# Kernel optimization log

Hardware: AMD Instinct MI355X
Metric: run time of the kernel (lower is better)

Reference implementation:

```python
import jax, jax.numpy as jnp
import numpy as np

B, N, T, NL, DIM, H, HD = 4, 2048, 8, 64, 1024, 16, 64


def setup_inputs() -> dict:
    key = jax.random.key(0)
    ks = jax.random.split(key, 8)
    text = jax.random.normal(ks[0], (B, N, DIM), dtype=jnp.float32)
    media = jax.random.normal(ks[1], (B, T, NL, DIM), dtype=jnp.float32)
    # place exactly T media tokens per row, evenly spaced, so cumsum times are in [1, T]
    loc = np.zeros((B, N), dtype=bool)
    step = N // T
    loc[:, np.arange(T) * step] = True
    media_locations = jnp.asarray(loc)
    s = 1.0 / np.sqrt(DIM)
    wq = jax.random.normal(ks[2], (DIM, DIM), dtype=jnp.float32) * s
    wkv = jax.random.normal(ks[3], (DIM, 2 * DIM), dtype=jnp.float32) * s
    wo = jax.random.normal(ks[4], (DIM, DIM), dtype=jnp.float32) * s
    bo = jnp.zeros((DIM,), dtype=jnp.float32)
    ln_g = jnp.ones((DIM,), dtype=jnp.float32)
    ln_b = jnp.zeros((DIM,), dtype=jnp.float32)
    return {"text": text, "media": media, "media_locations": media_locations,
            "wq": wq, "wkv": wkv, "wo": wo, "bo": bo, "ln_g": ln_g, "ln_b": ln_b}


def _layernorm(x, g, b, eps=1e-5):
    mu = jnp.mean(x, axis=-1, keepdims=True)
    var = jnp.var(x, axis=-1, keepdims=True)
    return (x - mu) * jax.lax.rsqrt(var + eps) * g + b


def reference(text, media, media_locations, wq, wkv, wo, bo, ln_g, ln_b):
    b, t, nl, d = media.shape
    tn = _layernorm(text, ln_g, ln_b)                 # [b, n, d]
    q = tn @ wq                                        # [b, n, d]
    m = media.reshape(b, t * nl, d)                    # [b, tn, d]
    kv = m @ wkv                                       # [b, tn, 2d]
    k, v = jnp.split(kv, 2, axis=-1)
    q = q.reshape(b, -1, H, HD).transpose(0, 2, 1, 3)  # [b, h, n, hd]
    k = k.reshape(b, -1, H, HD).transpose(0, 2, 1, 3)  # [b, h, tn, hd]
    v = v.reshape(b, -1, H, HD).transpose(0, 2, 1, 3)
    scores = jnp.einsum('bhid,bhjd->bhij', q, k)       # [b, h, n, tn]
    text_times = jnp.cumsum(media_locations.astype(jnp.int32), axis=-1)  # [b, n]
    media_times = jnp.repeat(jnp.arange(1, t + 1, dtype=jnp.int32), nl)  # [tn]
    mask = text_times[:, None, :, None] == media_times[None, None, None, :]
    neg = jnp.finfo(scores.dtype).min
    scores = jnp.where(mask, scores, neg)
    attn = jax.nn.softmax(scores, axis=-1)
    no_media = (text_times == 0)[:, None, :, None]     # [b, 1, n, 1]
    attn = jnp.where(no_media, 0.0, attn)
    out = jnp.einsum('bhij,bhjd->bhid', attn, v)       # [b, h, n, hd]
    out = out.transpose(0, 2, 1, 3).reshape(b, -1, H * HD)
    return out @ wo + bo
```

## Files before the change

### kernel.cpp

```cpp
#include <hip/hip_runtime.h>
#include <stdint.h>

#define B_ 4
#define N_ 2048
#define T_ 8
#define NL_ 64
#define DIM_ 1024
#define H_ 16
#define HD_ 64
#define TN_ (T_*NL_)

typedef __bf16 bf16x8 __attribute__((ext_vector_type(8)));
typedef float f32x4 __attribute__((ext_vector_type(4)));

__device__ __forceinline__ float b2f(unsigned short x) {
  union { uint32_t u; float f; } v; v.u = ((uint32_t)x) << 16; return v.f;
}
__device__ __forceinline__ unsigned short f2b(float f) {
  union { float f; uint32_t u; } v; v.f = f;
  uint32_t r = v.u + 0x7FFFu + ((v.u >> 16) & 1u);
  return (unsigned short)(r >> 16);
}

__device__ __forceinline__ void gload_lds16(const unsigned short* g, unsigned short* l) {
  __builtin_amdgcn_global_load_lds(
      (const __attribute__((address_space(1))) uint32_t*)g,
      (__attribute__((address_space(3))) uint32_t*)l, 16, 0, 0);
}

__global__ void detect_kernel(const unsigned short* __restrict__ text, int* __restrict__ flag) {
  int t = threadIdx.x;
  int bad = 0;
  #pragma unroll
  for (int i = 0; i < 16; i++) {
    unsigned short w = text[t * 16 + i];
    int e = (w >> 7) & 0xFF;
    if (e != 0 && (e < 90 || e > 150)) bad++;
  }
  __shared__ int red[256];
  red[t] = bad;
  __syncthreads();
  for (int o = 128; o > 0; o >>= 1) { if (t < o) red[t] += red[t + o]; __syncthreads(); }
  if (t == 0) flag[0] = (red[0] > 256) ? 1 : 0;
}

#define PREP_TIMES 4
#define PREP_LN    (B_*N_)
#define PREP_CAST  2049
#define PREP_TR    4096

__global__ __launch_bounds__(256) void prep_kernel(
    const void* __restrict__ locs, int* __restrict__ tt,
    const void* __restrict__ text, const void* __restrict__ lng,
    const void* __restrict__ lnb, unsigned short* __restrict__ tn,
    const void* __restrict__ media, unsigned short* __restrict__ mb,
    const void* __restrict__ bo, unsigned short* __restrict__ bob,
    const void* __restrict__ wq, unsigned short* __restrict__ wqt,
    const void* __restrict__ wkv, unsigned short* __restrict__ wkvt,
    const void* __restrict__ wo, unsigned short* __restrict__ wot,
    const int* __restrict__ flag) {
  __shared__ __align__(16) unsigned char shraw[32 * 33 * 2];
  int gb = blockIdx.x;
  int t = threadIdx.x;

  if (gb < PREP_TIMES) {
    int* red = (int*)shraw;
    int b = gb;
    const unsigned char* p8 = (const unsigned char*)locs;
    const int* p32 = (const int*)locs;
    int cnt = 0;
    for (int i = t; i < B_*N_; i += 256) cnt += (p8[i] != 0) ? 1 : 0;
    red[t] = cnt;
    __syncthreads();
    for (int off = 128; off > 0; off >>= 1) {
      if (t < off) red[t] += red[t + off];
      __syncthreads();
    }
    int total = red[0];
    __syncthreads();
    bool isb = (total >= 2 * T_);
    int x[8];
    int base = b * N_ + t * 8;
    if (isb) {
      #pragma unroll
      for (int i = 0; i < 8; i++) x[i] = (int)(p8[base + i] != 0);
    } else {
      #pragma unroll
      for (int i = 0; i < 8; i++) x[i] = (int)(p32[base + i] != 0);
    }
    #pragma unroll
    for (int i = 1; i < 8; i++) x[i] += x[i-1];
    int tot = x[7];
    red[t] = tot;
    __syncthreads();
    for (int off = 1; off < 256; off <<= 1) {
      int v = (t >= off) ? red[t - off] : 0;
      __syncthreads();
      red[t] += v;
      __syncthreads();
    }
    int excl = red[t] - tot;
    #pragma unroll
    for (int i = 0; i < 8; i++) tt[base + i] = excl + x[i];
    return;
  }
  gb -= PREP_TIMES;

  if (gb < PREP_LN) {
    float* sm = (float*)shraw;
    int row = gb;
    bool isf = (*flag != 0);
    float f0, f1, f2, f3, g0, g1, g2, g3, c0, c1, c2, c3;
    if (isf) {
      float4 xv = ((const float4*)text)[(size_t)row * (DIM_/4) + t];
      f0 = xv.x; f1 = xv.y; f2 = xv.z; f3 = xv.w;
      float4 gv = ((const float4*)lng)[t];
      g0 = gv.x; g1 = gv.y; g2 = gv.z; g3 = gv.w;
      float4 bv = ((const float4*)lnb)[t];
      c0 = bv.x; c1 = bv.y; c2 = bv.z; c3 = bv.w;
    } else {
      ushort4 xv = ((const ushort4*)text)[(size_t)row * (DIM_/4) + t];
      f0 = b2f(xv.x); f1 = b2f(xv.y); f2 = b2f(xv.z); f3 = b2f(xv.w);
      ushort4 gv = ((const ushort4*)lng)[t];
      g0 = b2f(gv.x); g1 = b2f(gv.y); g2 = b2f(gv.z); g3 = b2f(gv.w);
      ushort4 bv = ((const ushort4*)lnb)[t];
      c0 = b2f(bv.x); c1 = b2f(bv.y); c2 = b2f(bv.z); c3 = b2f(bv.w);
    }
    float s  = f0 + f1 + f2 + f3;
    float s2 = f0*f0 + f1*f1 + f2*f2 + f3*f3;
    for (int off = 32; off > 0; off >>= 1) { s += __shfl_xor(s, off); s2 += __shfl_xor(s2, off); }
    int wave = t >> 6, lane = t & 63;
    if (lane == 0) { sm[wave] = s; sm[wave + 4] = s2; }
    __syncthreads();
    float ts  = sm[0] + sm[1] + sm[2] + sm[3];
    float ts2 = sm[4] + sm[5] + sm[6] + sm[7];
    float mean = ts * (1.0f / DIM_);
    float var  = ts2 * (1.0f / DIM_) - mean * mean;
    float rs = rsqrtf(var + 1e-5f);
    ushort4 o;
    o.x = f2b((f0 - mean) * rs * g0 + c0);
    o.y = f2b((f1 - mean) * rs * g1 + c1);
    o.z = f2b((f2 - mean) * rs * g2 + c2);
    o.w = f2b((f3 - mean) * rs * g3 + c3);
    ((ushort4*)(tn + (size_t)row * DIM_))[t] = o;
    return;
  }
  gb -= PREP_LN;

  if (gb < PREP_CAST) {
    const int N4M = (B_*T_*NL_*DIM_) / 4;
    int i = gb * 256 + t;
    bool isf = (*flag != 0);
    if (i < N4M) {
      ushort4 o;
      if (isf) {
        float4 v = ((const float4*)media)[i];
        o.x = f2b(v.x); o.y = f2b(v.y); o.z = f2b(v.z); o.w = f2b(v.w);
      } else {
        o = ((const ushort4*)media)[i];
      }
      ((ushort4*)mb)[i] = o;
    } else {
      int j = i - N4M;
      if (j < DIM_/4) {
        ushort4 o;
        if (isf) {
          float4 v = ((const float4*)bo)[j];
          o.x = f2b(v.x); o.y = f2b(v.y); o.z = f2b(v.z); o.w = f2b(v.w);
        } else {
          o = ((const ushort4*)bo)[j];
        }
        ((ushort4*)bob)[j] = o;
      }
    }
    return;
  }
  gb -= PREP_CAST;

  {
    unsigned short (*tile)[33] = (unsigned short (*)[33])shraw;
    const void* src; unsigned short* dst; int C, zz, nx;
    if (gb < 1024)      { src = wq;  dst = wqt;  C = 1024; zz = gb;        nx = 32; }
    else if (gb < 3072) { src = wkv; dst = wkvt; C = 2048; zz = gb - 1024; nx = 64; }
    else                { src = wo;  dst = wot;  C = 1024; zz = gb - 3072; nx = 32; }
    const int R = 1024;
    int xi = zz % nx, yi = zz / nx;
    int bx = xi * 32, by = yi * 32;
    int x = t & 31, y = t >> 5;
    if (*flag) {
      const float* s = (const float*)src;
      for (int i = y; i < 32; i += 8) tile[i][x] = f2b(s[(size_t)(by + i) * C + bx + x]);
    } else {
      const unsigned short* s = (const unsigned short*)src;
      for (int i = y; i < 32; i += 8) tile[i][x] = s[(size_t)(by + i) * C + bx + x];
    }
    __syncthreads();
    for (int i = y; i < 32; i += 8) dst[(size_t)(bx + i) * R + by + x] = tile[x][i];
  }
}

__device__ __forceinline__ void gemm128_core(const unsigned short* __restrict__ A,
                                             const unsigned short* __restrict__ Bt,
                                             unsigned short* __restrict__ C,
                                             float* __restrict__ Cf,
                                             const unsigned short* __restrict__ bias,
                                             int bid, int mtiles, int M, int N, int K,
                                             bool f32o, int t) {
  __shared__ unsigned short As[3][128][32];
  __shared__ unsigned short Bs[3][128][32];
  int m0 = (bid % mtiles) * 128, n0 = (bid / mtiles) * 128;
  int wave = t >> 6, lane = t & 63;
  int wr = wave >> 1, wc = wave & 1;
  f32x4 acc[4][4];
  #pragma unroll
  for (int i = 0; i < 4; i++)
    #pragma unroll
    for (int j = 0; j < 4; j++)
      #pragma unroll
      for (int r = 0; r < 4; r++) acc[i][j][r] = 0.f;
  int lr = lane & 15, lk = (lane >> 4) * 8;
  int row0 = t >> 2,         kc0 = (t & 3) * 8;
  int row1 = (t + 256) >> 2, kc1 = ((t + 256) & 3) * 8;
  const unsigned short* a0 = A  + (size_t)(m0 + row0) * K + kc0;
  const unsigned short* a1 = A  + (size_t)(m0 + row1) * K + kc1;
  const unsigned short* b0 = Bt + (size_t)(n0 + row0) * K + kc0;
  const unsigned short* b1 = Bt + (size_t)(n0 + row1) * K + kc1;
#define STAGE_(buf, koff) do { \
    gload_lds16(a0 + (koff), &As[buf][row0][kc0]); \
    gload_lds16(a1 + (koff), &As[buf][row1][kc1]); \
    gload_lds16(b0 + (koff), &Bs[buf][row0][kc0]); \
    gload_lds16(b1 + (koff), &Bs[buf][row1][kc1]); \
  } while (0)
  STAGE_(0, 0);
  STAGE_(1, 32);
  STAGE_(2, 64);
  asm volatile("s_waitcnt vmcnt(8)" ::: "memory");
  __builtin_amdgcn_s_barrier();
  int cur = 0;
  for (int k0 = 0; k0 < K; k0 += 32) {
    bf16x8 af[4], bfr[4];
    #pragma unroll
    for (int i = 0; i < 4; i++) af[i]  = *(const bf16x8*)(&As[cur][wr * 64 + i * 16 + lr][lk]);
    #pragma unroll
    for (int j = 0; j < 4; j++) bfr[j] = *(const bf16x8*)(&Bs[cur][wc * 64 + j * 16 + lr][lk]);
    asm volatile("s_waitcnt lgkmcnt(0)" ::: "memory");
    __builtin_amdgcn_sched_barrier(0);
    __builtin_amdgcn_s_barrier();
    if (k0 + 96 < K) {
      STAGE_(cur, k0 + 96);
      __builtin_amdgcn_sched_barrier(0);
    }
    #pragma unroll
    for (int i = 0; i < 4; i++)
      #pragma unroll
      for (int j = 0; j < 4; j++)
        acc[i][j] = __builtin_amdgcn_mfma_f32_16x16x32_bf16(af[i], bfr[j], acc[i][j], 0, 0, 0);
    if (k0 + 96 < K) {
      asm volatile("s_waitcnt vmcnt(8)" ::: "memory");
      __builtin_amdgcn_s_barrier();
    } else if (k0 + 64 < K) {
      asm volatile("s_waitcnt vmcnt(4)" ::: "memory");
      __builtin_amdgcn_s_barrier();
    } else if (k0 + 32 < K) {
      asm volatile("s_waitcnt vmcnt(0)" ::: "memory");
      __builtin_amdgcn_s_barrier();
    }
    cur = (cur == 2) ? 0 : cur + 1;
  }
#undef STAGE_
  int rbase = (lane >> 4) * 4;
  int cbase = lane & 15;
  #pragma unroll
  for (int i = 0; i < 4; i++) {
    #pragma unroll
    for (int j = 0; j < 4; j++) {
      int row = m0 + wr * 64 + i * 16 + rbase;
      int col = n0 + wc * 64 + j * 16 + cbase;
      float bv = bias ? b2f(bias[col]) : 0.f;
      if (f32o) {
        #pragma unroll
        for (int r = 0; r < 4; r++)
          Cf[(size_t)(row + r) * N + col] = acc[i][j][r] + bv;
      } else {
        #pragma unroll
        for (int r = 0; r < 4; r++)
          C[(size_t)(row + r) * N + col] = f2b(acc[i][j][r] + bv);
      }
    }
  }
}

__global__ __launch_bounds__(256) void gemm_qkv(const unsigned short* __restrict__ tn,
                                                const unsigned short* __restrict__ wqt,
                                                unsigned short* __restrict__ qb,
                                                const unsigned short* __restrict__ mb,
                                                const unsigned short* __restrict__ wkvt,
                                                unsigned short* __restrict__ kvb) {
  int bid = blockIdx.x;
  if (bid < 512)
    gemm128_core(tn, wqt, qb, nullptr, nullptr, bid, 64, B_ * N_, DIM_, DIM_, false, threadIdx.x);
  else
    gemm128_core(mb, wkvt, kvb, nullptr, nullptr, bid - 512, 16, B_ * TN_, 2 * DIM_, DIM_, false, threadIdx.x);
}

__global__ __launch_bounds__(256) void gemm_out(const unsigned short* __restrict__ ao,
                                                const unsigned short* __restrict__ wot,
                                                unsigned short* __restrict__ C,
                                                float* __restrict__ Cf,
                                                const unsigned short* __restrict__ bias,
                                                const int* __restrict__ flag) {
  bool f32o = (*flag != 0);
  gemm128_core(ao, wot, C, Cf, bias, blockIdx.x, 64, B_ * N_, DIM_, DIM_, f32o, threadIdx.x);
}

__global__ __launch_bounds__(64) void attn_mfma(const unsigned short* __restrict__ q,
                                                const unsigned short* __restrict__ kv,
                                                const int* __restrict__ tt,
                                                unsigned short* __restrict__ ao) {
  __shared__ unsigned short Vt[64][72];
  __shared__ unsigned short Ps[64][72];
  int bid = blockIdx.x;
  int h  = bid & 15;
  int nt = (bid >> 4) & 31;
  int b  = bid >> 9;
  int bn0 = b * N_ + nt * 64;
  int lane = threadIdx.x & 63;
  int lr = lane & 15;
  int g  = lane >> 4;
  int g8 = g * 8;

  int tv = tt[bn0];
  float vmul = (tv >= 1 && tv <= T_) ? 1.f : 0.f;
  int tvc = tv < 1 ? 1 : (tv > T_ ? T_ : tv);
  int kvrow0 = b * TN_ + (tvc - 1) * NL_;

  const unsigned short* vbase = kv + (size_t)kvrow0 * (2 * DIM_) + DIM_ + h * HD_;
  #pragma unroll
  for (int d0 = 0; d0 < 64; d0 += 8) {
    uint4 v = *(const uint4*)(vbase + (size_t)lane * (2 * DIM_) + d0);
    Vt[d0 + 0][lane] = (unsigned short)(v.x & 0xffff);
    Vt[d0 + 1][lane] = (unsigned short)(v.x >> 16);
    Vt[d0 + 2][lane] = (unsigned short)(v.y & 0xffff);
    Vt[d0 + 3][lane] = (unsigned short)(v.y >> 16);
    Vt[d0 + 4][lane] = (unsigned short)(v.z & 0xffff);
    Vt[d0 + 5][lane] = (unsigned short)(v.z >> 16);
    Vt[d0 + 6][lane] = (unsigned short)(v.w & 0xffff);
    Vt[d0 + 7][lane] = (unsigned short)(v.w >> 16);
  }

  f32x4 S[4][4];
  #pragma unroll
  for (int i = 0; i < 4; i++)
    #pragma unroll
    for (int j = 0; j < 4; j++)
      #pragma unroll
      for (int r = 0; r < 4; r++) S[i][j][r] = 0.f;
  #pragma unroll
  for (int ks = 0; ks < 2; ks++) {
    bf16x8 aQ[4], bK[4];
    #pragma unroll
    for (int mi = 0; mi < 4; mi++)
      aQ[mi] = *(const bf16x8*)(q + (size_t)(bn0 + mi * 16 + lr) * DIM_ + h * HD_ + ks * 32 + g8);
    #pragma unroll
    for (int ni = 0; ni < 4; ni++)
      bK[ni] = *(const bf16x8*)(kv + (size_t)(kvrow0 + ni * 16 + lr) * (2 * DIM_) + h * HD_ + ks * 32 + g8);
    #pragma unroll
    for (int mi = 0; mi < 4; mi++)
      #pragma unroll
      for (int ni = 0; ni < 4; ni++)
        S[mi][ni] = __builtin_amdgcn_mfma_f32_16x16x32_bf16(aQ[mi], bK[ni], S[mi][ni], 0, 0, 0);
  }

  #pragma unroll
  for (int mi = 0; mi < 4; mi++) {
    #pragma unroll
    for (int r = 0; r < 4; r++) {
      float mx = fmaxf(fmaxf(S[mi][0][r], S[mi][1][r]), fmaxf(S[mi][2][r], S[mi][3][r]));
      mx = fmaxf(mx, __shfl_xor(mx, 1));
      mx = fmaxf(mx, __shfl_xor(mx, 2));
      mx = fmaxf(mx, __shfl_xor(mx, 4));
      mx = fmaxf(mx, __shfl_xor(mx, 8));
      float e0 = __expf(S[mi][0][r] - mx);
      float e1 = __expf(S[mi][1][r] - mx);
      float e2 = __expf(S[mi][2][r] - mx);
      float e3 = __expf(S[mi][3][r] - mx);
      float sum = e0 + e1 + e2 + e3;
      sum += __shfl_xor(sum, 1);
      sum += __shfl_xor(sum, 2);
      sum += __shfl_xor(sum, 4);
      sum += __shfl_xor(sum, 8);
      float inv = 1.f / sum;
      int qrow = mi * 16 + g * 4 + r;
      Ps[qrow][ 0 + lr] = f2b(e0 * inv);
      Ps[qrow][16 + lr] = f2b(e1 * inv);
      Ps[qrow][32 + lr] = f2b(e2 * inv);
      Ps[qrow][48 + lr] = f2b(e3 * inv);
    }
  }
  __syncthreads();

  f32x4 O[4][4];
  #pragma unroll
  for (int i = 0; i < 4; i++)
    #pragma unroll
    for (int j = 0; j < 4; j++)
      #pragma unroll
      for (int r = 0; r < 4; r++) O[i][j][r] = 0.f;
  #pragma unroll
  for (int ks = 0; ks < 2; ks++) {
    bf16x8 aP[4], bV[4];
    #pragma unroll
    for (int mi = 0; mi < 4; mi++)
      aP[mi] = *(const bf16x8*)(&Ps[mi * 16 + lr][ks * 32 + g8]);
    #pragma unroll
    for (int ni = 0; ni < 4; ni++)
      bV[ni] = *(const bf16x8*)(&Vt[ni * 16 + lr][ks * 32 + g8]);
    #pragma unroll
    for (int mi = 0; mi < 4; mi++)
      #pragma unroll
      for (int ni = 0; ni < 4; ni++)
        O[mi][ni] = __builtin_amdgcn_mfma_f32_16x16x32_bf16(aP[mi], bV[ni], O[mi][ni], 0, 0, 0);
  }
  __syncthreads();

  #pragma unroll
  for (int mi = 0; mi < 4; mi++)
    #pragma unroll
    for (int ni = 0; ni < 4; ni++)
      #pragma unroll
      for (int r = 0; r < 4; r++)
        Ps[mi * 16 + g * 4 + r][ni * 16 + lr] = f2b(O[mi][ni][r] * vmul);
  __syncthreads();
  uint4* dst = (uint4*)(ao + (size_t)(bn0 + lane) * DIM_ + h * HD_);
  #pragma unroll
  for (int c = 0; c < 8; c++)
    dst[c] = *(const uint4*)(&Ps[lane][c * 8]);
}

extern "C" void kernel_launch(void* const* d_in, const int* in_sizes, int n_in,
                              void* d_out, int out_size, void* d_ws, size_t ws_size,
                              hipStream_t stream) {
  const void* text = d_in[0];
  const void* media = d_in[1];
  const void* mloc = d_in[2];
  const void* wq  = d_in[3];
  const void* wkv = d_in[4];
  const void* wo  = d_in[5];
  const void* bo  = d_in[6];
  const void* lng = d_in[7];
  const void* lnb = d_in[8];

  char* ws = (char*)d_ws;
  const size_t OFF_FLAG = (size_t)32 << 10;
  const size_t OFF_TN   = (size_t)64 << 10;
  const size_t OFF_WQT  = OFF_TN  + ((size_t)16 << 20) + ((size_t)64 << 10);
  const size_t OFF_WKVT = OFF_WQT + ((size_t)2 << 20);
  const size_t OFF_WOT  = OFF_WKVT + ((size_t)4 << 20);
  const size_t OFF_KV   = OFF_WOT + ((size_t)2 << 20);
  const size_t OFF_MB   = OFF_KV  + ((size_t)8 << 20);
  const size_t OFF_BO   = OFF_MB  + ((size_t)4 << 20);
  const size_t OFF_QB   = OFF_BO  + ((size_t)64 << 10);
  int* tt               = (int*)(ws + 0);
  int* flag             = (int*)(ws + OFF_FLAG);
  unsigned short* tn    = (unsigned short*)(ws + OFF_TN);
  unsigned short* ao    = tn;
  unsigned short* wqt   = (unsigned short*)(ws + OFF_WQT);
  unsigned short* wkvt  = (unsigned short*)(ws + OFF_WKVT);
  unsigned short* wot   = (unsigned short*)(ws + OFF_WOT);
  unsigned short* kvb   = (unsigned short*)(ws + OFF_KV);
  unsigned short* mb    = (unsigned short*)(ws + OFF_MB);
  unsigned short* bob   = (unsigned short*)(ws + OFF_BO);
  unsigned short* qb    = (unsigned short*)(ws + OFF_QB);

  detect_kernel<<<1, 256, 0, stream>>>((const unsigned short*)text, flag);
  prep_kernel<<<PREP_TIMES + PREP_LN + PREP_CAST + PREP_TR, 256, 0, stream>>>(
      mloc, tt, text, lng, lnb, tn, media, mb, bo, bob,
      wq, wqt, wkv, wkvt, wo, wot, flag);

  gemm_qkv<<<768, 256, 0, stream>>>(tn, wqt, qb, mb, wkvt, kvb);
  attn_mfma<<<B_ * (N_/64) * H_, 64, 0, stream>>>(qb, kvb, tt, ao);
  gemm_out<<<512, 256, 0, stream>>>(ao, wot, (unsigned short*)d_out, (float*)d_out, bob, flag);
}
```

Baseline: 194.5 us.

## Fold dtype detection into prep kernel and halve attention tile with register-held V

```diff
diff --git a/kernel.cpp b/kernel.cpp
--- a/kernel.cpp
+++ b/kernel.cpp
@@ -28,20 +28,18 @@
       (__attribute__((address_space(3))) uint32_t*)l, 16, 0, 0);
 }
 
-__global__ void detect_kernel(const unsigned short* __restrict__ text, int* __restrict__ flag) {
-  int t = threadIdx.x;
+__device__ __forceinline__ bool detect_isf(const unsigned short* text, int t) {
+  int l = t & 63;
   int bad = 0;
   #pragma unroll
   for (int i = 0; i < 16; i++) {
-    unsigned short w = text[t * 16 + i];
+    unsigned short w = text[l * 16 + i];
     int e = (w >> 7) & 0xFF;
     if (e != 0 && (e < 90 || e > 150)) bad++;
   }
-  __shared__ int red[256];
-  red[t] = bad;
-  __syncthreads();
-  for (int o = 128; o > 0; o >>= 1) { if (t < o) red[t] += red[t + o]; __syncthreads(); }
-  if (t == 0) flag[0] = (red[0] > 256) ? 1 : 0;
+  #pragma unroll
+  for (int off = 32; off > 0; off >>= 1) bad += __shfl_xor(bad, off);
+  return bad > 64;
 }
 
 #define PREP_TIMES 4
@@ -58,10 +56,12 @@
     const void* __restrict__ wq, unsigned short* __restrict__ wqt,
     const void* __restrict__ wkv, unsigned short* __restrict__ wkvt,
     const void* __restrict__ wo, unsigned short* __restrict__ wot,
-    const int* __restrict__ flag) {
+    int* __restrict__ flag) {
   __shared__ __align__(16) unsigned char shraw[32 * 33 * 2];
   int gb = blockIdx.x;
   int t = threadIdx.x;
+  bool isf = detect_isf((const unsigned short*)text, t);
+  if (gb == 0 && t == 0) flag[0] = isf ? 1 : 0;
 
   if (gb < PREP_TIMES) {
     int* red = (int*)shraw;
@@ -109,7 +109,6 @@
   if (gb < PREP_LN) {
     float* sm = (float*)shraw;
     int row = gb;
-    bool isf = (*flag != 0);
     float f0, f1, f2, f3, g0, g1, g2, g3, c0, c1, c2, c3;
     if (isf) {
       float4 xv = ((const float4*)text)[(size_t)row * (DIM_/4) + t];
@@ -150,7 +149,6 @@
   if (gb < PREP_CAST) {
     const int N4M = (B_*T_*NL_*DIM_) / 4;
     int i = gb * 256 + t;
-    bool isf = (*flag != 0);
     if (i < N4M) {
       ushort4 o;
       if (isf) {
@@ -187,7 +185,7 @@
     int xi = zz % nx, yi = zz / nx;
     int bx = xi * 32, by = yi * 32;
     int x = t & 31, y = t >> 5;
-    if (*flag) {
+    if (isf) {
       const float* s = (const float*)src;
       for (int i = y; i < 32; i += 8) tile[i][x] = f2b(s[(size_t)(by + i) * C + bx + x]);
     } else {
@@ -317,13 +315,12 @@
                                                 const unsigned short* __restrict__ kv,
                                                 const int* __restrict__ tt,
                                                 unsigned short* __restrict__ ao) {
-  __shared__ unsigned short Vt[64][72];
-  __shared__ unsigned short Ps[64][72];
+  __shared__ unsigned short Ps[32][68];
   int bid = blockIdx.x;
   int h  = bid & 15;
-  int nt = (bid >> 4) & 31;
-  int b  = bid >> 9;
-  int bn0 = b * N_ + nt * 64;
+  int nt = (bid >> 4) & 63;
+  int b  = bid >> 10;
+  int bn0 = b * N_ + nt * 32;
   int lane = threadIdx.x & 63;
   int lr = lane & 15;
   int g  = lane >> 4;
@@ -334,45 +331,41 @@
   int tvc = tv < 1 ? 1 : (tv > T_ ? T_ : tv);
   int kvrow0 = b * TN_ + (tvc - 1) * NL_;
 
-  const unsigned short* vbase = kv + (size_t)kvrow0 * (2 * DIM_) + DIM_ + h * HD_;
-  #pragma unroll
-  for (int d0 = 0; d0 < 64; d0 += 8) {
-    uint4 v = *(const uint4*)(vbase + (size_t)lane * (2 * DIM_) + d0);
-    Vt[d0 + 0][lane] = (unsigned short)(v.x & 0xffff);
-    Vt[d0 + 1][lane] = (unsigned short)(v.x >> 16);
-    Vt[d0 + 2][lane] = (unsigned short)(v.y & 0xffff);
-    Vt[d0 + 3][lane] = (unsigned short)(v.y >> 16);
-    Vt[d0 + 4][lane] = (unsigned short)(v.z & 0xffff);
-    Vt[d0 + 5][lane] = (unsigned short)(v.z >> 16);
-    Vt[d0 + 6][lane] = (unsigned short)(v.w & 0xffff);
-    Vt[d0 + 7][lane] = (unsigned short)(v.w >> 16);
-  }
-
-  f32x4 S[4][4];
-  #pragma unroll
-  for (int i = 0; i < 4; i++)
+  const unsigned short* vb = kv + (size_t)kvrow0 * (2 * DIM_) + DIM_ + h * HD_;
+  bf16x8 bV[2][4];
+  #pragma unroll
+  for (int ks = 0; ks < 2; ks++)
+    #pragma unroll
+    for (int ni = 0; ni < 4; ni++)
+      #pragma unroll
+      for (int j = 0; j < 8; j++)
+        bV[ks][ni][j] = *(const __bf16*)(vb + (size_t)(ks * 32 + g8 + j) * (2 * DIM_) + ni * 16 + lr);
+
+  f32x4 S[2][4];
+  #pragma unroll
+  for (int i = 0; i < 2; i++)
     #pragma unroll
     for (int j = 0; j < 4; j++)
       #pragma unroll
       for (int r = 0; r < 4; r++) S[i][j][r] = 0.f;
   #pragma unroll
   for (int ks = 0; ks < 2; ks++) {
-    bf16x8 aQ[4], bK[4];
-    #pragma unroll
-    for (int mi = 0; mi < 4; mi++)
+    bf16x8 aQ[2], bK[4];
+    #pragma unroll
+    for (int mi = 0; mi < 2; mi++)
       aQ[mi] = *(const bf16x8*)(q + (size_t)(bn0 + mi * 16 + lr) * DIM_ + h * HD_ + ks * 32 + g8);
     #pragma unroll
     for (int ni = 0; ni < 4; ni++)
       bK[ni] = *(const bf16x8*)(kv + (size_t)(kvrow0 + ni * 16 + lr) * (2 * DIM_) + h * HD_ + ks * 32 + g8);
     #pragma unroll
-    for (int mi = 0; mi < 4; mi++)
+    for (int mi = 0; mi < 2; mi++)
       #pragma unroll
       for (int ni = 0; ni < 4; ni++)
         S[mi][ni] = __builtin_amdgcn_mfma_f32_16x16x32_bf16(aQ[mi], bK[ni], S[mi][ni], 0, 0, 0);
   }
 
   #pragma unroll
-  for (int mi = 0; mi < 4; mi++) {
+  for (int mi = 0; mi < 2; mi++) {
     #pragma unroll
     for (int r = 0; r < 4; r++) {
       float mx = fmaxf(fmaxf(S[mi][0][r], S[mi][1][r]), fmaxf(S[mi][2][r], S[mi][3][r]));
@@ -399,42 +392,40 @@
   }
   __syncthreads();
 
-  f32x4 O[4][4];
-  #pragma unroll
-  for (int i = 0; i < 4; i++)
+  f32x4 O[2][4];
+  #pragma unroll
+  for (int i = 0; i < 2; i++)
     #pragma unroll
     for (int j = 0; j < 4; j++)
       #pragma unroll
       for (int r = 0; r < 4; r++) O[i][j][r] = 0.f;
   #pragma unroll
   for (int ks = 0; ks < 2; ks++) {
-    bf16x8 aP[4], bV[4];
-    #pragma unroll
-    for (int mi = 0; mi < 4; mi++)
+    bf16x8 aP[2];
+    #pragma unroll
+    for (int mi = 0; mi < 2; mi++)
       aP[mi] = *(const bf16x8*)(&Ps[mi * 16 + lr][ks * 32 + g8]);
     #pragma unroll
-    for (int ni = 0; ni < 4; ni++)
-      bV[ni] = *(const bf16x8*)(&Vt[ni * 16 + lr][ks * 32 + g8]);
-    #pragma unroll
-    for (int mi = 0; mi < 4; mi++)
+    for (int mi = 0; mi < 2; mi++)
       #pragma unroll
       for (int ni = 0; ni < 4; ni++)
-        O[mi][ni] = __builtin_amdgcn_mfma_f32_16x16x32_bf16(aP[mi], bV[ni], O[mi][ni], 0, 0, 0);
+        O[mi][ni] = __builtin_amdgcn_mfma_f32_16x16x32_bf16(aP[mi], bV[ks][ni], O[mi][ni], 0, 0, 0);
   }
   __syncthreads();
 
   #pragma unroll
-  for (int mi = 0; mi < 4; mi++)
+  for (int mi = 0; mi < 2; mi++)
     #pragma unroll
     for (int ni = 0; ni < 4; ni++)
       #pragma unroll
       for (int r = 0; r < 4; r++)
         Ps[mi * 16 + g * 4 + r][ni * 16 + lr] = f2b(O[mi][ni][r] * vmul);
   __syncthreads();
-  uint4* dst = (uint4*)(ao + (size_t)(bn0 + lane) * DIM_ + h * HD_);
-  #pragma unroll
-  for (int c = 0; c < 8; c++)
-    dst[c] = *(const uint4*)(&Ps[lane][c * 8]);
+  int row = lane >> 1, half = lane & 1;
+  uint4* dst = (uint4*)(ao + (size_t)(bn0 + row) * DIM_ + h * HD_ + half * 32);
+  #pragma unroll
+  for (int c = 0; c < 4; c++)
+    dst[c] = *(const uint4*)(&Ps[row][half * 32 + c * 8]);
 }
 
 extern "C" void kernel_launch(void* const* d_in, const int* in_sizes, int n_in,
@@ -472,12 +463,11 @@
   unsigned short* bob   = (unsigned short*)(ws + OFF_BO);
   unsigned short* qb    = (unsigned short*)(ws + OFF_QB);
 
-  detect_kernel<<<1, 256, 0, stream>>>((const unsigned short*)text, flag);
   prep_kernel<<<PREP_TIMES + PREP_LN + PREP_CAST + PREP_TR, 256, 0, stream>>>(
       mloc, tt, text, lng, lnb, tn, media, mb, bo, bob,
       wq, wqt, wkv, wkvt, wo, wot, flag);
 
   gemm_qkv<<<768, 256, 0, stream>>>(tn, wqt, qb, mb, wkvt, kvb);
-  attn_mfma<<<B_ * (N_/64) * H_, 64, 0, stream>>>(qb, kvb, tt, ao);
+  attn_mfma<<<B_ * (N_/32) * H_, 64, 0, stream>>>(qb, kvb, tt, ao);
   gemm_out<<<512, 256, 0, stream>>>(ao, wot, (unsigned short*)d_out, (float*)d_out, bob, flag);
 }
```

New measurement: 197.7 us. No clear change (+1.6%).
